# Kernel optimization log

Measured on AMD Instinct MI355X. Metric: run time of the kernel, lower is better.

Reference implementation:

```python
import jax, jax.numpy as jnp
import numpy as np

B, M, L, S = 16, 128, 32, 512
D, H, DFF, NL = 768, 12, 3072, 4
NE = 50000
HD = D // H
EPS = 1e-5


def _ln(x, w, b):
    mu = jnp.mean(x, axis=-1, keepdims=True)
    var = jnp.var(x, axis=-1, keepdims=True)
    return (x - mu) * jax.lax.rsqrt(var + EPS) * w + b


def setup_inputs() -> dict:
    key = jax.random.key(0)
    ks = jax.random.split(key, 24)
    sd = 0.02
    lens = jax.random.randint(ks[1], (B, M), 1, L + 1)
    pos = jax.random.randint(ks[2], (B, M, L), 0, S)
    pos = jnp.where(jnp.arange(L)[None, None, :] < lens[..., None], pos, -1)
    return {
        "last_hidden_state": jax.random.normal(ks[0], (B, S, D), jnp.float32),
        "entity_position_ids": pos.astype(jnp.int64),
        "entity_attention_mask": jax.random.randint(ks[3], (B, M), 0, 2).astype(jnp.int64),
        "attn_w": jax.random.normal(ks[4], (D,), jnp.float32) * sd,
        "attn_b": jnp.zeros((), jnp.float32),
        "qkv_w": jax.random.normal(ks[5], (NL, 3 * D, D), jnp.float32) * sd,
        "qkv_b": jnp.zeros((NL, 3 * D), jnp.float32),
        "out_w": jax.random.normal(ks[6], (NL, D, D), jnp.float32) * sd,
        "out_b": jnp.zeros((NL, D), jnp.float32),
        "ln1_w": jnp.ones((NL, D), jnp.float32),
        "ln1_b": jnp.zeros((NL, D), jnp.float32),
        "ff1_w": jax.random.normal(ks[7], (NL, DFF, D), jnp.float32) * sd,
        "ff1_b": jnp.zeros((NL, DFF), jnp.float32),
        "ff2_w": jax.random.normal(ks[8], (NL, D, DFF), jnp.float32) * sd,
        "ff2_b": jnp.zeros((NL, D), jnp.float32),
        "ln2_w": jnp.ones((NL, D), jnp.float32),
        "ln2_b": jnp.zeros((NL, D), jnp.float32),
        "cls_w1": jax.random.normal(ks[9], (100, D), jnp.float32) * sd,
        "cls_w2": jax.random.normal(ks[10], (NE, 100), jnp.float32) * sd,
        "cls_b2": jnp.zeros((NE,), jnp.float32),
    }


def reference(last_hidden_state, entity_position_ids, entity_attention_mask,
              attn_w, attn_b, qkv_w, qkv_b, out_w, out_b, ln1_w, ln1_b,
              ff1_w, ff1_b, ff2_w, ff2_b, ln2_w, ln2_b, cls_w1, cls_w2, cls_b2):
    # Ragged mention fill (vectorized form of the triple python loop).
    # Original code writes last_hidden_state[i, x, :] (loop index x, not the
    # position id) until the first -1 in entity_position_ids[i, j, :].
    not_break = jnp.cumprod((entity_position_ids != -1).astype(jnp.int32), axis=-1)  # [B,M,L]
    valid = (entity_attention_mask != 0)[:, :, None].astype(jnp.int32) * not_break   # [B,M,L]
    mentions = valid[..., None].astype(last_hidden_state.dtype) * \
        last_hidden_state[:, None, :L, :]  # [B,M,L,D]

    # attention pooling over mention length
    logits = jnp.einsum('bmld,d->bml', mentions, attn_w) + attn_b
    scores = jax.nn.softmax(logits, axis=-1)
    x = jnp.einsum('bml,bmld->bmd', scores, mentions)  # [B,M,D]

    scale = 1.0 / np.sqrt(HD)
    for i in range(NL):
        qkv = x @ qkv_w[i].T + qkv_b[i]  # [B,M,3D]
        q, k, v = jnp.split(qkv, 3, axis=-1)
        q = q.reshape(B, M, H, HD).transpose(0, 2, 1, 3)
        k = k.reshape(B, M, H, HD).transpose(0, 2, 1, 3)
        v = v.reshape(B, M, H, HD).transpose(0, 2, 1, 3)
        attn = jax.nn.softmax(jnp.einsum('bhqd,bhkd->bhqk', q, k) * scale, axis=-1)
        ao = jnp.einsum('bhqk,bhkd->bhqd', attn, v).transpose(0, 2, 1, 3).reshape(B, M, D)
        ao = ao @ out_w[i].T + out_b[i]
        x = _ln(x + ao, ln1_w[i], ln1_b[i])
        ff = jax.nn.relu(x @ ff1_w[i].T + ff1_b[i]) @ ff2_w[i].T + ff2_b[i]
        x = _ln(x + ff, ln2_w[i], ln2_b[i])

    return (x @ cls_w1.T) @ cls_w2.T + cls_b2  # [B,M,NE]
```

## Files before the change

kernel.cpp:

```cpp
#include <hip/hip_runtime.h>
#include <math.h>

#define NBATCH 16
#define NMENT  128
#define NM     2048
#define LSEQ   32
#define SSEQ   512
#define DD     768
#define NHEAD  12
#define HDIM   64
#define DFF    3072
#define NLAYER 4
#define NENT   50000

typedef __bf16 bf16;
typedef __attribute__((__ext_vector_type__(4))) float f32x4;
typedef __attribute__((__ext_vector_type__(8))) bf16 bf16x8;
typedef __attribute__((__ext_vector_type__(4))) bf16 bf16x4;

__device__ __forceinline__ void gl2lds16(const bf16* g, bf16* l) {
  __builtin_amdgcn_global_load_lds(
      (const __attribute__((address_space(1))) void*)g,
      (__attribute__((address_space(3))) void*)l, 16, 0, 0);
}

__global__ __launch_bounds__(256) void conv_bf16(const float* __restrict__ s,
                                                 bf16* __restrict__ d, int n4) {
  const int i = blockIdx.x * 256 + threadIdx.x;
  if (i >= n4) return;
  const float4 v = ((const float4*)s)[i];
  bf16x4 o;
  o.x = (bf16)v.x; o.y = (bf16)v.y; o.z = (bf16)v.z; o.w = (bf16)v.w;
  ((bf16x4*)d)[i] = o;
}

__global__ __launch_bounds__(256) void conv_pad(const float* __restrict__ s,
                                                bf16* __restrict__ d,
                                                int srows, int scols, int dcols,
                                                int total) {
  const int i = blockIdx.x * 256 + threadIdx.x;
  if (i >= total) return;
  const int r = i / dcols, c = i - r * dcols;
  const float v = (r < srows && c < scols) ? s[(size_t)r * scols + c] : 0.f;
  d[i] = (bf16)v;
}

__global__ __launch_bounds__(256) void red4_bf16(const float* __restrict__ p,
                                                 bf16* __restrict__ d, int n4) {
  const int i = blockIdx.x * 256 + threadIdx.x;
  if (i >= n4) return;
  const float4 a = ((const float4*)p)[i];
  const float4 b = ((const float4*)p)[i + (size_t)n4];
  const float4 c = ((const float4*)p)[i + 2 * (size_t)n4];
  const float4 e = ((const float4*)p)[i + 3 * (size_t)n4];
  bf16x4 o;
  o.x = (bf16)(a.x + b.x + c.x + e.x);
  o.y = (bf16)(a.y + b.y + c.y + e.y);
  o.z = (bf16)(a.z + b.z + c.z + e.z);
  o.w = (bf16)(a.w + b.w + c.w + e.w);
  ((bf16x4*)d)[i] = o;
}

__global__ __launch_bounds__(64) void tdot_kernel(const float* __restrict__ lhs,
                                                  const float* __restrict__ aw,
                                                  float* __restrict__ t) {
  const int bl = blockIdx.x;
  const int b = bl >> 5, l = bl & 31;
  const int lane = threadIdx.x;
  const float* row = lhs + ((size_t)b * SSEQ + l) * DD;
  float s = 0.f;
#pragma unroll
  for (int u = 0; u < DD / 64; ++u)
    s += row[lane + 64 * u] * aw[lane + 64 * u];
#pragma unroll
  for (int off = 32; off > 0; off >>= 1) s += __shfl_down(s, off);
  if (lane == 0) t[bl] = s;
}

__global__ __launch_bounds__(256) void pool_kernel(const float* __restrict__ lhs,
                                                   const int* __restrict__ pos,
                                                   const int* __restrict__ msk,
                                                   const float* __restrict__ t,
                                                   float* __restrict__ X,
                                                   bf16* __restrict__ Xb) {
  __shared__ float wgt[LSEQ];
  __shared__ int ok[LSEQ];
  const int bm = blockIdx.x;
  const int b = bm >> 7;
  const int tid = threadIdx.x;
  if (tid < LSEQ) ok[tid] = (pos[(size_t)bm * LSEQ + tid] != -1) ? 1 : 0;
  __syncthreads();
  if (tid == 0) {
    const int mk = (msk[bm] != 0) ? 1 : 0;
    int run = 1;
    float lg[LSEQ];
    int vld[LSEQ];
#pragma unroll
    for (int l = 0; l < LSEQ; ++l) {
      run &= ok[l];
      vld[l] = mk & run;
      lg[l] = vld[l] ? t[b * LSEQ + l] : 0.f;
    }
    float mx = lg[0];
#pragma unroll
    for (int l = 1; l < LSEQ; ++l) mx = fmaxf(mx, lg[l]);
    float s = 0.f;
#pragma unroll
    for (int l = 0; l < LSEQ; ++l) { lg[l] = expf(lg[l] - mx); s += lg[l]; }
    const float inv = 1.f / s;
#pragma unroll
    for (int l = 0; l < LSEQ; ++l) wgt[l] = vld[l] ? lg[l] * inv : 0.f;
  }
  __syncthreads();
#pragma unroll
  for (int u = 0; u < 3; ++u) {
    const int d = tid + 256 * u;
    float acc = 0.f;
#pragma unroll
    for (int l = 0; l < LSEQ; ++l)
      acc += wgt[l] * lhs[((size_t)b * SSEQ + l) * DD + d];
    X[(size_t)bm * DD + d] = acc;
    Xb[(size_t)bm * DD + d] = (bf16)acc;
  }
}

template <int OUT_BF16, int RELU, int HAS_BIAS, int GUARD_N>
__global__ __launch_bounds__(256) void gemm_mfma(const bf16* __restrict__ A,
                                                 const bf16* __restrict__ B,
                                                 const float* __restrict__ bias,
                                                 void* __restrict__ Cp,
                                                 int K, int lda, int ldb,
                                                 int ldc, int ncols) {
  __shared__ __align__(16) bf16 As[128 * 32];
  __shared__ __align__(16) bf16 Bs[128 * 32];
  const int tid = threadIdx.x;
  const int wave = tid >> 6, lane = tid & 63;
  const int rb = blockIdx.y * 128, cb = blockIdx.x * 128;
  const int wm = (wave >> 1) * 64, wn = (wave & 1) * 64;
  const int koff = blockIdx.z * K;

  const int sr = wave * 32 + (lane >> 2);
  const int sk = (lane & 3) * 8;
  const bf16* ga0 = A + (size_t)(rb + sr) * lda + koff + sk;
  const bf16* ga1 = A + (size_t)(rb + sr + 16) * lda + koff + sk;
  const bf16* gb0 = B + (size_t)(cb + sr) * ldb + koff + sk;
  const bf16* gb1 = B + (size_t)(cb + sr + 16) * ldb + koff + sk;
  bf16* sa0 = As + wave * 1024;
  bf16* sa1 = As + wave * 1024 + 512;
  bf16* sb0 = Bs + wave * 1024;
  bf16* sb1 = Bs + wave * 1024 + 512;

  const int fr = lane & 15, fk = (lane >> 4) * 8;

  f32x4 acc[4][4];
#pragma unroll
  for (int i = 0; i < 4; ++i)
#pragma unroll
    for (int j = 0; j < 4; ++j) acc[i][j] = (f32x4)0.f;

  for (int kb = 0; kb < K; kb += 32) {
    gl2lds16(ga0, sa0); gl2lds16(ga1, sa1);
    gl2lds16(gb0, sb0); gl2lds16(gb1, sb1);
    ga0 += 32; ga1 += 32; gb0 += 32; gb1 += 32;
    __syncthreads();
    bf16x8 af[4], bfr[4];
#pragma unroll
    for (int i = 0; i < 4; ++i)
      af[i] = *(const bf16x8*)(As + (wm + i * 16 + fr) * 32 + fk);
#pragma unroll
    for (int j = 0; j < 4; ++j)
      bfr[j] = *(const bf16x8*)(Bs + (wn + j * 16 + fr) * 32 + fk);
#pragma unroll
    for (int i = 0; i < 4; ++i)
#pragma unroll
      for (int j = 0; j < 4; ++j)
        acc[i][j] = __builtin_amdgcn_mfma_f32_16x16x32_bf16(af[i], bfr[j],
                                                            acc[i][j], 0, 0, 0);
    __syncthreads();
  }

  const size_t zoff = (size_t)blockIdx.z * (size_t)(gridDim.y << 7) * ldc;
  const int r0 = rb + wm + ((lane >> 4) << 2);
  const int c0 = cb + wn + fr;
#pragma unroll
  for (int i = 0; i < 4; ++i) {
#pragma unroll
    for (int j = 0; j < 4; ++j) {
      const int col = c0 + j * 16;
      if (GUARD_N && col >= ncols) continue;
      const float bv = HAS_BIAS ? bias[col] : 0.f;
#pragma unroll
      for (int r = 0; r < 4; ++r) {
        float v = acc[i][j][r] + bv;
        if (RELU) v = fmaxf(v, 0.f);
        const int row = r0 + i * 16 + r;
        if (OUT_BF16)
          ((bf16*)Cp)[zoff + (size_t)row * ldc + col] = (bf16)v;
        else
          ((float*)Cp)[zoff + (size_t)row * ldc + col] = v;
      }
    }
  }
}

__global__ __launch_bounds__(256) void attn_kernel(const float* __restrict__ qkv,
                                                   bf16* __restrict__ ao) {
  __shared__ float smem[2 * 64 * 132 + 128 * 132];
  float* Qs = smem;
  float* Ks = smem + 64 * 132;
  float* Ps = smem + 2 * 64 * 132;
  float* Vs = smem;

  const int tid = threadIdx.x;
  const int b = blockIdx.x / NHEAD;
  const int h = blockIdx.x % NHEAD;
  const float* base = qkv + (size_t)b * NMENT * (3 * DD) + h * HDIM;

#pragma unroll
  for (int it = 0; it < 8; ++it) {
    const int idx = tid + it * 256;
    const int m = idx >> 4;
    const int d0 = (idx & 15) * 4;
    const float4 q = *(const float4*)(base + (size_t)m * (3 * DD) + d0);
    const float4 k = *(const float4*)(base + (size_t)m * (3 * DD) + DD + d0);
    Qs[(d0 + 0) * 132 + m] = q.x; Qs[(d0 + 1) * 132 + m] = q.y;
    Qs[(d0 + 2) * 132 + m] = q.z; Qs[(d0 + 3) * 132 + m] = q.w;
    Ks[(d0 + 0) * 132 + m] = k.x; Ks[(d0 + 1) * 132 + m] = k.y;
    Ks[(d0 + 2) * 132 + m] = k.z; Ks[(d0 + 3) * 132 + m] = k.w;
  }
  __syncthreads();

  const int tm = (tid >> 4) * 8;
  const int tn = (tid & 15) * 8;
  {
    float acc[8][8];
#pragma unroll
    for (int i = 0; i < 8; ++i)
#pragma unroll
      for (int j = 0; j < 8; ++j) acc[i][j] = 0.f;
    for (int d = 0; d < HDIM; ++d) {
      float a[8], bv[8];
      *(float4*)&a[0] = *(const float4*)&Qs[d * 132 + tm];
      *(float4*)&a[4] = *(const float4*)&Qs[d * 132 + tm + 4];
      *(float4*)&bv[0] = *(const float4*)&Ks[d * 132 + tn];
      *(float4*)&bv[4] = *(const float4*)&Ks[d * 132 + tn + 4];
#pragma unroll
      for (int i = 0; i < 8; ++i)
#pragma unroll
        for (int j = 0; j < 8; ++j)
          acc[i][j] = fmaf(a[i], bv[j], acc[i][j]);
    }
    const float scale = 0.125f;
#pragma unroll
    for (int i = 0; i < 8; ++i)
#pragma unroll
      for (int j = 0; j < 8; ++j)
        Ps[(tn + j) * 132 + (tm + i)] = acc[i][j] * scale;
  }
  __syncthreads();

#pragma unroll
  for (int it = 0; it < 8; ++it) {
    const int idx = tid + it * 256;
    const int m = idx >> 4;
    const int d0 = (idx & 15) * 4;
    const float4 v = *(const float4*)(base + (size_t)m * (3 * DD) + 2 * DD + d0);
    *(float4*)&Vs[m * 68 + d0] = v;
  }
  if (tid < NMENT) {
    const int r = tid;
    float mx = -1e30f;
    for (int c = 0; c < NMENT; ++c) mx = fmaxf(mx, Ps[c * 132 + r]);
    float s = 0.f;
    for (int c = 0; c < NMENT; ++c) {
      const float e = expf(Ps[c * 132 + r] - mx);
      Ps[c * 132 + r] = e;
      s += e;
    }
    const float inv = 1.f / s;
    for (int c = 0; c < NMENT; ++c) Ps[c * 132 + r] *= inv;
  }
  __syncthreads();

  const int om = (tid >> 4) * 8;
  const int od = (tid & 15) * 4;
  float oacc[8][4];
#pragma unroll
  for (int i = 0; i < 8; ++i)
#pragma unroll
    for (int j = 0; j < 4; ++j) oacc[i][j] = 0.f;
  for (int c = 0; c < NMENT; ++c) {
    float p[8];
    *(float4*)&p[0] = *(const float4*)&Ps[c * 132 + om];
    *(float4*)&p[4] = *(const float4*)&Ps[c * 132 + om + 4];
    const float4 vv = *(const float4*)&Vs[c * 68 + od];
#pragma unroll
    for (int i = 0; i < 8; ++i) {
      oacc[i][0] = fmaf(p[i], vv.x, oacc[i][0]);
      oacc[i][1] = fmaf(p[i], vv.y, oacc[i][1]);
      oacc[i][2] = fmaf(p[i], vv.z, oacc[i][2]);
      oacc[i][3] = fmaf(p[i], vv.w, oacc[i][3]);
    }
  }
#pragma unroll
  for (int i = 0; i < 8; ++i) {
    bf16x4 ov;
    ov.x = (bf16)oacc[i][0]; ov.y = (bf16)oacc[i][1];
    ov.z = (bf16)oacc[i][2]; ov.w = (bf16)oacc[i][3];
    *(bf16x4*)(ao + (size_t)(b * NMENT + om + i) * DD + h * HDIM + od) = ov;
  }
}

template <int NS>
__global__ __launch_bounds__(256) void ln_kernel(const float* __restrict__ x,
                                                 const float* __restrict__ y,
                                                 const float* __restrict__ bias,
                                                 const float* __restrict__ w,
                                                 const float* __restrict__ bb,
                                                 float* __restrict__ o,
                                                 bf16* __restrict__ ob) {
  __shared__ float red1[4], red2[4];
  __shared__ float mshare, vshare;
  const int row = blockIdx.x;
  const int tid = threadIdx.x;
  const int wave = tid >> 6, lane = tid & 63;
  const float* xr = x + (size_t)row * DD;
  const float* yr = y + (size_t)row * DD;
  float v[3];
  float s = 0.f;
#pragma unroll
  for (int u = 0; u < 3; ++u) {
    const int d = tid + 256 * u;
    float acc = xr[d] + bias[d];
#pragma unroll
    for (int n = 0; n < NS; ++n) acc += yr[(size_t)n * NM * DD + d];
    v[u] = acc;
    s += acc;
  }
#pragma unroll
  for (int off = 32; off > 0; off >>= 1) s += __shfl_down(s, off);
  if (lane == 0) red1[wave] = s;
  __syncthreads();
  if (tid == 0) mshare = (red1[0] + red1[1] + red1[2] + red1[3]) * (1.f / DD);
  __syncthreads();
  const float mean = mshare;
  float q = 0.f;
#pragma unroll
  for (int u = 0; u < 3; ++u) { const float d = v[u] - mean; q += d * d; }
#pragma unroll
  for (int off = 32; off > 0; off >>= 1) q += __shfl_down(q, off);
  if (lane == 0) red2[wave] = q;
  __syncthreads();
  if (tid == 0)
    vshare = rsqrtf((red2[0] + red2[1] + red2[2] + red2[3]) * (1.f / DD) + 1e-5f);
  __syncthreads();
  const float rstd = vshare;
  float* orow = o + (size_t)row * DD;
  bf16* brow = ob + (size_t)row * DD;
#pragma unroll
  for (int u = 0; u < 3; ++u) {
    const int d = tid + 256 * u;
    const float r = (v[u] - mean) * rstd * w[d] + bb[d];
    orow[d] = r;
    brow[d] = (bf16)r;
  }
}

extern "C" void kernel_launch(void* const* d_in, const int* in_sizes, int n_in,
                              void* d_out, int out_size, void* d_ws, size_t ws_size,
                              hipStream_t stream) {
  const float* lhs    = (const float*)d_in[0];
  const int*   pos    = (const int*)d_in[1];
  const int*   msk    = (const int*)d_in[2];
  const float* attn_w = (const float*)d_in[3];
  const float* qkv_w  = (const float*)d_in[5];
  const float* qkv_b  = (const float*)d_in[6];
  const float* out_w  = (const float*)d_in[7];
  const float* out_b  = (const float*)d_in[8];
  const float* ff1_w  = (const float*)d_in[11];
  const float* ff1_b  = (const float*)d_in[12];
  const float* ff2_w  = (const float*)d_in[13];
  const float* ff2_b  = (const float*)d_in[14];
  const float* ln1_w  = (const float*)d_in[9];
  const float* ln1_b  = (const float*)d_in[10];
  const float* ln2_w  = (const float*)d_in[15];
  const float* ln2_b  = (const float*)d_in[16];
  const float* cls_w1 = (const float*)d_in[17];
  const float* cls_w2 = (const float*)d_in[18];
  const float* cls_b2 = (const float*)d_in[19];
  float* out = (float*)d_out;

  char* p = (char*)d_ws;
  auto carve = [&](size_t bytes) {
    void* r = (void*)p;
    p += (bytes + 255) & ~(size_t)255;
    return r;
  };
  float* T    = (float*)carve(512 * 4);
  float* X    = (float*)carve((size_t)NM * DD * 4);
  float* SCR  = (float*)carve((size_t)4 * NM * DD * 4);
  bf16* Xb    = (bf16*)carve((size_t)NM * DD * 2);
  bf16* AOb   = (bf16*)carve((size_t)NM * DD * 2);
  bf16* H1    = (bf16*)carve((size_t)NM * DFF * 2);
  bf16* Hb    = (bf16*)carve((size_t)NM * 128 * 2);
  bf16* Wqkv  = (bf16*)carve((size_t)NLAYER * 3 * DD * DD * 2);
  bf16* Wout  = (bf16*)carve((size_t)NLAYER * DD * DD * 2);
  bf16* Wff1  = (bf16*)carve((size_t)NLAYER * DFF * DD * 2);
  bf16* Wff2  = (bf16*)carve((size_t)NLAYER * DD * DFF * 2);
  bf16* Wc1   = (bf16*)carve((size_t)128 * DD * 2);
  bf16* Wc2   = (bf16*)carve((size_t)50048 * 128 * 2);

  {
    const int n_qkv = NLAYER * 3 * DD * DD / 4;
    const int n_out = NLAYER * DD * DD / 4;
    const int n_ff  = NLAYER * DFF * DD / 4;
    conv_bf16<<<(n_qkv + 255) / 256, 256, 0, stream>>>(qkv_w, Wqkv, n_qkv);
    conv_bf16<<<(n_out + 255) / 256, 256, 0, stream>>>(out_w, Wout, n_out);
    conv_bf16<<<(n_ff + 255) / 256, 256, 0, stream>>>(ff1_w, Wff1, n_ff);
    conv_bf16<<<(n_ff + 255) / 256, 256, 0, stream>>>(ff2_w, Wff2, n_ff);
    const int t1 = 128 * DD;
    const int t2 = 50048 * 128;
    conv_pad<<<(t1 + 255) / 256, 256, 0, stream>>>(cls_w1, Wc1, 100, DD, DD, t1);
    conv_pad<<<(t2 + 255) / 256, 256, 0, stream>>>(cls_w2, Wc2, NENT, 100, 128, t2);
  }

  tdot_kernel<<<NBATCH * LSEQ, 64, 0, stream>>>(lhs, attn_w, T);
  pool_kernel<<<NM, 256, 0, stream>>>(lhs, pos, msk, T, X, Xb);

  for (int i = 0; i < NLAYER; ++i) {
    gemm_mfma<0, 0, 1, 0><<<dim3(18, 16), 256, 0, stream>>>(
        Xb, Wqkv + (size_t)i * 3 * DD * DD, qkv_b + (size_t)i * 3 * DD, SCR,
        DD, DD, DD, 3 * DD, 3 * DD);
    attn_kernel<<<NBATCH * NHEAD, 256, 0, stream>>>(SCR, AOb);
    gemm_mfma<0, 0, 0, 0><<<dim3(6, 16, 2), 256, 0, stream>>>(
        AOb, Wout + (size_t)i * DD * DD, nullptr, SCR,
        DD / 2, DD, DD, DD, DD);
    ln_kernel<2><<<NM, 256, 0, stream>>>(X, SCR, out_b + (size_t)i * DD,
                                         ln1_w + (size_t)i * DD,
                                         ln1_b + (size_t)i * DD, X, Xb);
    gemm_mfma<1, 1, 1, 0><<<dim3(24, 16), 256, 0, stream>>>(
        Xb, Wff1 + (size_t)i * DFF * DD, ff1_b + (size_t)i * DFF, H1,
        DD, DD, DD, DFF, DFF);
    gemm_mfma<0, 0, 0, 0><<<dim3(6, 16, 4), 256, 0, stream>>>(
        H1, Wff2 + (size_t)i * DD * DFF, nullptr, SCR,
        DFF / 4, DFF, DFF, DD, DD);
    ln_kernel<4><<<NM, 256, 0, stream>>>(X, SCR, ff2_b + (size_t)i * DD,
                                         ln2_w + (size_t)i * DD,
                                         ln2_b + (size_t)i * DD, X, Xb);
  }

  gemm_mfma<0, 0, 0, 0><<<dim3(1, 16, 4), 256, 0, stream>>>(
      Xb, Wc1, nullptr, SCR, DD / 4, DD, DD, 128, 128);
  {
    const int n4 = NM * 128 / 4;
    red4_bf16<<<(n4 + 255) / 256, 256, 0, stream>>>(SCR, Hb, n4);
  }
  gemm_mfma<0, 0, 1, 1><<<dim3(391, 16), 256, 0, stream>>>(
      Hb, Wc2, cls_b2, out, 128, 128, 128, NENT, NENT);
}
```

Measured before the change: 1.164 ms.

## Double-buffer LDS tiles in MFMA GEMM and fuse weight conversion kernels

Measured after the change: 1.121 ms. 1.04x faster.

```diff
diff --git a/kernel.cpp b/kernel.cpp
--- a/kernel.cpp
+++ b/kernel.cpp
@@ -24,25 +24,46 @@
       (__attribute__((address_space(3))) void*)l, 16, 0, 0);
 }
 
-__global__ __launch_bounds__(256) void conv_bf16(const float* __restrict__ s,
-                                                 bf16* __restrict__ d, int n4) {
-  const int i = blockIdx.x * 256 + threadIdx.x;
-  if (i >= n4) return;
+#define C_QKV (NLAYER * 3 * DD * DD / 4)
+#define C_OUT (NLAYER * DD * DD / 4)
+#define C_FF  (NLAYER * DFF * DD / 4)
+#define C_W1  (128 * DD)
+#define C_W2  (50048 * 128)
+#define C_TOTAL (C_QKV + C_OUT + 2 * C_FF + C_W1 + C_W2)
+
+__device__ __forceinline__ void cvt4(const float* s, bf16* d, int i) {
   const float4 v = ((const float4*)s)[i];
   bf16x4 o;
   o.x = (bf16)v.x; o.y = (bf16)v.y; o.z = (bf16)v.z; o.w = (bf16)v.w;
   ((bf16x4*)d)[i] = o;
 }
 
-__global__ __launch_bounds__(256) void conv_pad(const float* __restrict__ s,
-                                                bf16* __restrict__ d,
-                                                int srows, int scols, int dcols,
-                                                int total) {
-  const int i = blockIdx.x * 256 + threadIdx.x;
-  if (i >= total) return;
-  const int r = i / dcols, c = i - r * dcols;
-  const float v = (r < srows && c < scols) ? s[(size_t)r * scols + c] : 0.f;
-  d[i] = (bf16)v;
+__global__ __launch_bounds__(256) void conv_all(
+    const float* __restrict__ qkv_w, const float* __restrict__ out_w,
+    const float* __restrict__ ff1_w, const float* __restrict__ ff2_w,
+    const float* __restrict__ cls_w1, const float* __restrict__ cls_w2,
+    bf16* __restrict__ Wqkv, bf16* __restrict__ Wout, bf16* __restrict__ Wff1,
+    bf16* __restrict__ Wff2, bf16* __restrict__ Wc1, bf16* __restrict__ Wc2) {
+  int i = blockIdx.x * 256 + threadIdx.x;
+  if (i < C_QKV) { cvt4(qkv_w, Wqkv, i); return; }
+  i -= C_QKV;
+  if (i < C_OUT) { cvt4(out_w, Wout, i); return; }
+  i -= C_OUT;
+  if (i < C_FF) { cvt4(ff1_w, Wff1, i); return; }
+  i -= C_FF;
+  if (i < C_FF) { cvt4(ff2_w, Wff2, i); return; }
+  i -= C_FF;
+  if (i < C_W1) {
+    const int r = i / DD;
+    Wc1[i] = (bf16)((r < 100) ? cls_w1[i] : 0.f);
+    return;
+  }
+  i -= C_W1;
+  if (i < C_W2) {
+    const int r = i >> 7, c = i & 127;
+    const float v = (r < NENT && c < 100) ? cls_w2[r * 100 + c] : 0.f;
+    Wc2[i] = (bf16)v;
+  }
 }
 
 __global__ __launch_bounds__(256) void red4_bf16(const float* __restrict__ p,
@@ -131,8 +152,8 @@
                                                  void* __restrict__ Cp,
                                                  int K, int lda, int ldb,
                                                  int ldc, int ncols) {
-  __shared__ __align__(16) bf16 As[128 * 32];
-  __shared__ __align__(16) bf16 Bs[128 * 32];
+  __shared__ __align__(16) bf16 As[2][128 * 32];
+  __shared__ __align__(16) bf16 Bs[2][128 * 32];
   const int tid = threadIdx.x;
   const int wave = tid >> 6, lane = tid & 63;
   const int rb = blockIdx.y * 128, cb = blockIdx.x * 128;
@@ -145,10 +166,7 @@
   const bf16* ga1 = A + (size_t)(rb + sr + 16) * lda + koff + sk;
   const bf16* gb0 = B + (size_t)(cb + sr) * ldb + koff + sk;
   const bf16* gb1 = B + (size_t)(cb + sr + 16) * ldb + koff + sk;
-  bf16* sa0 = As + wave * 1024;
-  bf16* sa1 = As + wave * 1024 + 512;
-  bf16* sb0 = Bs + wave * 1024;
-  bf16* sb1 = Bs + wave * 1024 + 512;
+  const int so = wave * 1024;
 
   const int fr = lane & 15, fk = (lane >> 4) * 8;
 
@@ -158,18 +176,28 @@
 #pragma unroll
     for (int j = 0; j < 4; ++j) acc[i][j] = (f32x4)0.f;
 
-  for (int kb = 0; kb < K; kb += 32) {
-    gl2lds16(ga0, sa0); gl2lds16(ga1, sa1);
-    gl2lds16(gb0, sb0); gl2lds16(gb1, sb1);
-    ga0 += 32; ga1 += 32; gb0 += 32; gb1 += 32;
-    __syncthreads();
+  gl2lds16(ga0, &As[0][so]); gl2lds16(ga1, &As[0][so + 512]);
+  gl2lds16(gb0, &Bs[0][so]); gl2lds16(gb1, &Bs[0][so + 512]);
+  ga0 += 32; ga1 += 32; gb0 += 32; gb1 += 32;
+  __syncthreads();
+
+  const int nsteps = K >> 5;
+  int cur = 0;
+  for (int t = 0; t < nsteps; ++t) {
+    if (t + 1 < nsteps) {
+      const int nxt = cur ^ 1;
+      gl2lds16(ga0, &As[nxt][so]); gl2lds16(ga1, &As[nxt][so + 512]);
+      gl2lds16(gb0, &Bs[nxt][so]); gl2lds16(gb1, &Bs[nxt][so + 512]);
+      ga0 += 32; ga1 += 32; gb0 += 32; gb1 += 32;
+    }
+    __builtin_amdgcn_sched_barrier(0);
     bf16x8 af[4], bfr[4];
 #pragma unroll
     for (int i = 0; i < 4; ++i)
-      af[i] = *(const bf16x8*)(As + (wm + i * 16 + fr) * 32 + fk);
+      af[i] = *(const bf16x8*)(&As[cur][(wm + i * 16 + fr) * 32 + fk]);
 #pragma unroll
     for (int j = 0; j < 4; ++j)
-      bfr[j] = *(const bf16x8*)(Bs + (wn + j * 16 + fr) * 32 + fk);
+      bfr[j] = *(const bf16x8*)(&Bs[cur][(wn + j * 16 + fr) * 32 + fk]);
 #pragma unroll
     for (int i = 0; i < 4; ++i)
 #pragma unroll
@@ -177,6 +205,7 @@
         acc[i][j] = __builtin_amdgcn_mfma_f32_16x16x32_bf16(af[i], bfr[j],
                                                             acc[i][j], 0, 0, 0);
     __syncthreads();
+    cur ^= 1;
   }
 
   const size_t zoff = (size_t)blockIdx.z * (size_t)(gridDim.y << 7) * ldc;
@@ -410,19 +439,9 @@
   bf16* Wc1   = (bf16*)carve((size_t)128 * DD * 2);
   bf16* Wc2   = (bf16*)carve((size_t)50048 * 128 * 2);
 
-  {
-    const int n_qkv = NLAYER * 3 * DD * DD / 4;
-    const int n_out = NLAYER * DD * DD / 4;
-    const int n_ff  = NLAYER * DFF * DD / 4;
-    conv_bf16<<<(n_qkv + 255) / 256, 256, 0, stream>>>(qkv_w, Wqkv, n_qkv);
-    conv_bf16<<<(n_out + 255) / 256, 256, 0, stream>>>(out_w, Wout, n_out);
-    conv_bf16<<<(n_ff + 255) / 256, 256, 0, stream>>>(ff1_w, Wff1, n_ff);
-    conv_bf16<<<(n_ff + 255) / 256, 256, 0, stream>>>(ff2_w, Wff2, n_ff);
-    const int t1 = 128 * DD;
-    const int t2 = 50048 * 128;
-    conv_pad<<<(t1 + 255) / 256, 256, 0, stream>>>(cls_w1, Wc1, 100, DD, DD, t1);
-    conv_pad<<<(t2 + 255) / 256, 256, 0, stream>>>(cls_w2, Wc2, NENT, 100, 128, t2);
-  }
+  conv_all<<<(C_TOTAL + 255) / 256, 256, 0, stream>>>(
+      qkv_w, out_w, ff1_w, ff2_w, cls_w1, cls_w2,
+      Wqkv, Wout, Wff1, Wff2, Wc1, Wc2);
 
   tdot_kernel<<<NBATCH * LSEQ, 64, 0, stream>>>(lhs, attn_w, T);
   pool_kernel<<<NM, 256, 0, stream>>>(lhs, pos, msk, T, X, Xb);
```
